# Kernel tuning notes

Hardware: AMD Instinct MI355X
Metric: run time of the kernel (lower is better)

## Reference

```python
import jax, jax.numpy as jnp
import numpy as np

N_HEADS = 4


def setup_inputs() -> dict:
    key = jax.random.key(0)
    k1, k2, k3 = jax.random.split(key, 3)
    B, C, H, W = 16, 512, 32, 32
    x = jax.random.normal(k1, (B, C, H, W), dtype=jnp.float32)
    # Linear weights stored as (in, out) so y = x @ w + b
    w_proj = jax.random.normal(k2, (C, 3 * C), dtype=jnp.float32) * (C ** -0.5)
    b_proj = jnp.zeros((3 * C,), dtype=jnp.float32)
    w_out = jax.random.normal(k3, (C, C), dtype=jnp.float32) * (C ** -0.5)
    b_out = jnp.zeros((C,), dtype=jnp.float32)
    return {"x": x, "w_proj": w_proj, "b_proj": b_proj, "w_out": w_out, "b_out": b_out}


def reference(x, w_proj, b_proj, w_out, b_out):
    B, C, H, W = x.shape
    d_k = C // N_HEADS
    scale = d_k ** -0.5
    # NOTE: original module defines GroupNorm but never applies it in forward.
    xf = x.reshape(B, C, H * W).transpose(0, 2, 1)          # (B, N, C)
    qkv = xf @ w_proj + b_proj                                # (B, N, 3C)
    qkv = qkv.reshape(B, -1, N_HEADS, 3 * d_k)
    q, k, v = jnp.split(qkv, 3, axis=-1)                      # each (B, N, H, d_k)
    attn = jnp.einsum('bihd,bjhd->bijh', q, k) * scale        # (B, N, N, H)
    attn = jax.nn.softmax(attn, axis=2)                       # softmax over j
    res = jnp.einsum('bijh,bjhd->bihd', attn, v)              # (B, N, H, d_k)
    res = res.reshape(B, -1, N_HEADS * d_k)                   # (B, N, C)
    res = res @ w_out + b_out + xf                            # residual add
    return res.transpose(0, 2, 1).reshape(B, C, H, W)
```

## Files before the change

kernel.cpp:

```cpp
#include <hip/hip_runtime.h>

#define B_  16
#define C_  512
#define N_  1024
#define NH  4
#define DK  128
#define M3  1536

typedef unsigned short u16;
typedef unsigned int   u32;
typedef __attribute__((ext_vector_type(8))) short bfrag;
typedef __attribute__((ext_vector_type(4))) float f4;

#define MFMA(a, b, c) __builtin_amdgcn_mfma_f32_16x16x32_bf16(a, b, c, 0, 0, 0)

#define GL2LDS(gp, lp) __builtin_amdgcn_global_load_lds( \
    (__attribute__((address_space(1))) const unsigned int*)(const void*)(gp), \
    (__attribute__((address_space(3))) unsigned int*)(void*)(lp), 16, 0, 0)

__device__ __forceinline__ u16 f2bf(float f) {
    u32 u = __float_as_uint(f);
    return (u16)((u + 0x7FFFu + ((u >> 16) & 1u)) >> 16);
}
__device__ __forceinline__ float bf2f(u16 h) { return __uint_as_float(((u32)h) << 16); }

#define QSCL 0.12751741859316937f

__global__ __launch_bounds__(256) void conv_split_t(
    const float* __restrict__ src, u16* __restrict__ dhi, u16* __restrict__ dlo,
    int R, int Cc)
{
    __shared__ float Ts[64][65];
    const int tid = threadIdx.x;
    const int c0 = blockIdx.x * 64, r0 = blockIdx.y * 64;
    const size_t bofs = (size_t)blockIdx.z * R * Cc;

#pragma unroll
    for (int p = 0; p < 4; ++p) {
        int r = p * 16 + (tid >> 4);
        int c = (tid & 15) * 4;
        float4 v = *(const float4*)(src + bofs + (size_t)(r0 + r) * Cc + c0 + c);
        Ts[c + 0][r] = v.x; Ts[c + 1][r] = v.y; Ts[c + 2][r] = v.z; Ts[c + 3][r] = v.w;
    }
    __syncthreads();
#pragma unroll
    for (int p = 0; p < 4; ++p) {
        int cc = p * 16 + (tid >> 4);
        int rr = (tid & 15) * 4;
        float f0 = Ts[cc][rr + 0], f1 = Ts[cc][rr + 1];
        float f2 = Ts[cc][rr + 2], f3 = Ts[cc][rr + 3];
        u16 h0 = f2bf(f0), h1 = f2bf(f1), h2 = f2bf(f2), h3 = f2bf(f3);
        u16 l0 = f2bf(f0 - bf2f(h0)), l1 = f2bf(f1 - bf2f(h1));
        u16 l2 = f2bf(f2 - bf2f(h2)), l3 = f2bf(f3 - bf2f(h3));
        size_t o = bofs + (size_t)(c0 + cc) * R + r0 + rr;
        *(uint2*)(void*)(dhi + o) = make_uint2((u32)h0 | ((u32)h1 << 16), (u32)h2 | ((u32)h3 << 16));
        *(uint2*)(void*)(dlo + o) = make_uint2((u32)l0 | ((u32)l1 << 16), (u32)l2 | ((u32)l3 << 16));
    }
}

__global__ __launch_bounds__(256, 2) void qkv_mfma(
    const u16* __restrict__ xt_hi, const u16* __restrict__ xt_lo,
    const u16* __restrict__ wpT_hi, const u16* __restrict__ wpT_lo,
    const float* __restrict__ bp,
    u16* __restrict__ Qh, u16* __restrict__ Ql,
    u16* __restrict__ Kh, u16* __restrict__ Kl,
    u16* __restrict__ Vth, u16* __restrict__ Vtl)
{
    __shared__ __align__(16) u16 AH[128 * 64], AL[128 * 64], BH[128 * 64], BL[128 * 64];
    const int tid = threadIdx.x;
    const int l = tid & 63, w = tid >> 6;
    const int wr = w >> 1, wc = w & 1;
    const int lm = l & 15, kg = l >> 4;
    const int bx = blockIdx.x, by = blockIdx.y, b = blockIdx.z;
    const int m0 = bx * 128, n0 = by * 128;

    const u16* gsrc =
        (w == 0) ? xt_hi + ((size_t)b * N_ + n0) * C_ :
        (w == 1) ? xt_lo + ((size_t)b * N_ + n0) * C_ :
        (w == 2) ? wpT_hi + (size_t)m0 * C_ :
                   wpT_lo + (size_t)m0 * C_;
    u16* ldst = (w == 0) ? AH : (w == 1) ? AL : (w == 2) ? BH : BL;
    const int lane_off = (l >> 3) * C_ + (((l & 7) ^ (l >> 3)) << 3);

    f4 acc[4][4] = {};

    for (int it = 0; it < 8; ++it) {
        __syncthreads();
        const u16* g = gsrc + it * 64 + lane_off;
#pragma unroll
        for (int u = 0; u < 16; ++u)
            GL2LDS(g + (size_t)u * 8 * C_, ldst + u * 512);
        __syncthreads();

#pragma unroll
        for (int kk = 0; kk < 2; ++kk) {
            bfrag ah[4], al[4], bh[4], bl[4];
            const int s = ((kk * 4 + kg) ^ (lm & 7)) << 3;
#pragma unroll
            for (int f = 0; f < 4; ++f) {
                const int ar = wr * 64 + f * 16 + lm;
                const int br = wc * 64 + f * 16 + lm;
                ah[f] = *(const bfrag*)(AH + ar * 64 + s);
                al[f] = *(const bfrag*)(AL + ar * 64 + s);
                bh[f] = *(const bfrag*)(BH + br * 64 + s);
                bl[f] = *(const bfrag*)(BL + br * 64 + s);
            }
#pragma unroll
            for (int i = 0; i < 4; ++i)
#pragma unroll
                for (int j = 0; j < 4; ++j) {
                    acc[i][j] = MFMA(ah[i], bh[j], acc[i][j]);
                    acc[i][j] = MFMA(ah[i], bl[j], acc[i][j]);
                    acc[i][j] = MFMA(al[i], bh[j], acc[i][j]);
                }
        }
    }

    const int hh = bx / 3, t = bx - hh * 3;
#pragma unroll
    for (int j = 0; j < 4; ++j) {
        const int mcol = m0 + wc * 64 + j * 16 + lm;
        const float bias = bp[mcol];
        const int d = mcol & 127;
#pragma unroll
        for (int i = 0; i < 4; ++i) {
            const int tok = n0 + wr * 64 + i * 16 + kg * 4;
            if (t == 2) {
                u16 hb[4], lb[4];
#pragma unroll
                for (int r = 0; r < 4; ++r) {
                    float v = acc[i][j][r] + bias;
                    hb[r] = f2bf(v);
                    lb[r] = f2bf(v - bf2f(hb[r]));
                }
                const size_t o = ((size_t)(b * NH + hh) * DK + d) * N_ + tok;
                *(uint2*)(void*)(Vth + o) = make_uint2((u32)hb[0] | ((u32)hb[1] << 16),
                                                       (u32)hb[2] | ((u32)hb[3] << 16));
                *(uint2*)(void*)(Vtl + o) = make_uint2((u32)lb[0] | ((u32)lb[1] << 16),
                                                       (u32)lb[2] | ((u32)lb[3] << 16));
            } else {
                u16* dh = (t == 0) ? Qh : Kh;
                u16* dl = (t == 0) ? Ql : Kl;
                const size_t o = ((size_t)(b * NH + hh) * N_ + tok) * DK + d;
#pragma unroll
                for (int r = 0; r < 4; ++r) {
                    float v = acc[i][j][r] + bias;
                    if (t == 0) v *= QSCL;
                    u16 hb = f2bf(v);
                    dh[o + (size_t)r * DK] = hb;
                    dl[o + (size_t)r * DK] = f2bf(v - bf2f(hb));
                }
            }
        }
    }
}

__global__ __launch_bounds__(512, 2) void attn_mfma(
    const u16* __restrict__ Qh_, const u16* __restrict__ Ql_,
    const u16* __restrict__ Kh_, const u16* __restrict__ Kl_,
    const u16* __restrict__ Vth_, const u16* __restrict__ Vtl_,
    u16* __restrict__ res_hi, u16* __restrict__ res_lo)
{
    __shared__ __align__(16) u16 KH[64 * 128], KL[64 * 128];
    __shared__ __align__(16) u16 VH[128 * 64], VL[128 * 64];
    __shared__ u16 Ph[8][2][16][72], Pl[8][2][16][72];

    const int tid = threadIdx.x;
    const int l = tid & 63, w = tid >> 6;
    const int lm = l & 15, kg = l >> 4;
    const int bh = blockIdx.x;
    const int qc = blockIdx.y;
    const int i0s = qc * 256 + w * 16 + lm;
    const size_t head = (size_t)bh * N_ * DK;

    const u16* sgK = (w & 2) ? Kl_ : Kh_;
    const u16* sgV = (w & 2) ? Vtl_ : Vth_;
    u16* sdK = (w & 2) ? KL : KH;
    u16* sdV = (w & 2) ? VL : VH;
    const int sub0 = (w & 1) * 8;

    bfrag qfh[2][4], qfl[2][4];
#pragma unroll
    for (int s = 0; s < 2; ++s) {
        const u16* qp  = Qh_ + head + (size_t)(i0s + s * 128) * DK + kg * 8;
        const u16* qp2 = Ql_ + head + (size_t)(i0s + s * 128) * DK + kg * 8;
#pragma unroll
        for (int kc = 0; kc < 4; ++kc) {
            qfh[s][kc] = *(const bfrag*)(qp + kc * 32);
            qfl[s][kc] = *(const bfrag*)(qp2 + kc * 32);
        }
    }

    f4 acc_o[2][8] = {};
    float m_r[2] = {-3.0e38f, -3.0e38f}, l_r[2] = {0.f, 0.f};

    for (int jt = 0; jt < 16; ++jt) {
        __syncthreads();
        if (w < 4) {
#pragma unroll
            for (int u = 0; u < 8; ++u) {
                const int rbase = (sub0 + u) * 4;
                const int row = rbase + (l >> 4);
                GL2LDS(sgK + head + (size_t)(jt * 64 + row) * DK + (((l & 15) ^ (row & 7)) << 3),
                       sdK + rbase * 128);
            }
        } else {
#pragma unroll
            for (int u = 0; u < 8; ++u) {
                const int rbase = (sub0 + u) * 8;
                const int row = rbase + (l >> 3);
                GL2LDS(sgV + (size_t)bh * DK * N_ + (size_t)row * N_ + jt * 64
                           + (((l & 7) ^ (row & 7)) << 3),
                       sdV + rbase * 64);
            }
        }
        __syncthreads();

        f4 sacc[2][4] = {};
#pragma unroll
        for (int kc = 0; kc < 4; ++kc) {
#pragma unroll
            for (int jf = 0; jf < 4; ++jf) {
                const int row = jf * 16 + lm;
                const int sw = (((kc << 2) | kg) ^ (lm & 7)) << 3;
                bfrag kh = *(const bfrag*)(KH + row * 128 + sw);
                bfrag kl = *(const bfrag*)(KL + row * 128 + sw);
#pragma unroll
                for (int s = 0; s < 2; ++s) {
                    sacc[s][jf] = MFMA(kh, qfh[s][kc], sacc[s][jf]);
                    sacc[s][jf] = MFMA(kh, qfl[s][kc], sacc[s][jf]);
                    sacc[s][jf] = MFMA(kl, qfh[s][kc], sacc[s][jf]);
                }
            }
        }

#pragma unroll
        for (int s = 0; s < 2; ++s) {
            float mt = sacc[s][0][0];
#pragma unroll
            for (int jf = 0; jf < 4; ++jf)
#pragma unroll
                for (int r = 0; r < 4; ++r) mt = fmaxf(mt, sacc[s][jf][r]);
            mt = fmaxf(mt, __shfl_xor(mt, 16));
            mt = fmaxf(mt, __shfl_xor(mt, 32));
            const float mn = fmaxf(m_r[s], mt);
            const float alpha = exp2f(m_r[s] - mn);
            m_r[s] = mn;

            float rs = 0.f;
#pragma unroll
            for (int jf = 0; jf < 4; ++jf) {
                u16 hb[4], lb[4];
#pragma unroll
                for (int r = 0; r < 4; ++r) {
                    float pv = exp2f(sacc[s][jf][r] - mn);
                    rs += pv;
                    hb[r] = f2bf(pv);
                    lb[r] = f2bf(pv - bf2f(hb[r]));
                }
                *(uint2*)(void*)&Ph[w][s][lm][jf * 16 + kg * 4] =
                    make_uint2((u32)hb[0] | ((u32)hb[1] << 16), (u32)hb[2] | ((u32)hb[3] << 16));
                *(uint2*)(void*)&Pl[w][s][lm][jf * 16 + kg * 4] =
                    make_uint2((u32)lb[0] | ((u32)lb[1] << 16), (u32)lb[2] | ((u32)lb[3] << 16));
            }
            rs += __shfl_xor(rs, 16);
            rs += __shfl_xor(rs, 32);
            l_r[s] = l_r[s] * alpha + rs;
#pragma unroll
            for (int df = 0; df < 8; ++df)
#pragma unroll
                for (int r = 0; r < 4; ++r) acc_o[s][df][r] *= alpha;
        }

#pragma unroll
        for (int kc2 = 0; kc2 < 2; ++kc2) {
            bfrag pbh0 = *(const bfrag*)&Ph[w][0][lm][kc2 * 32 + kg * 8];
            bfrag pbl0 = *(const bfrag*)&Pl[w][0][lm][kc2 * 32 + kg * 8];
            bfrag pbh1 = *(const bfrag*)&Ph[w][1][lm][kc2 * 32 + kg * 8];
            bfrag pbl1 = *(const bfrag*)&Pl[w][1][lm][kc2 * 32 + kg * 8];
#pragma unroll
            for (int df = 0; df < 8; ++df) {
                const int row = df * 16 + lm;
                const int sw = (((kc2 << 2) | kg) ^ (lm & 7)) << 3;
                bfrag vh = *(const bfrag*)(VH + row * 64 + sw);
                bfrag vl = *(const bfrag*)(VL + row * 64 + sw);
                acc_o[0][df] = MFMA(vh, pbh0, acc_o[0][df]);
                acc_o[0][df] = MFMA(vh, pbl0, acc_o[0][df]);
                acc_o[0][df] = MFMA(vl, pbh0, acc_o[0][df]);
                acc_o[1][df] = MFMA(vh, pbh1, acc_o[1][df]);
                acc_o[1][df] = MFMA(vh, pbl1, acc_o[1][df]);
                acc_o[1][df] = MFMA(vl, pbh1, acc_o[1][df]);
            }
        }
    }

    const int b = bh >> 2, h = bh & 3;
#pragma unroll
    for (int s = 0; s < 2; ++s) {
        const float inv = 1.f / l_r[s];
        const size_t ro = ((size_t)b * N_ + i0s + s * 128) * C_ + h * DK;
#pragma unroll
        for (int df = 0; df < 8; ++df) {
            u16 hb[4], lb[4];
#pragma unroll
            for (int r = 0; r < 4; ++r) {
                float v = acc_o[s][df][r] * inv;
                hb[r] = f2bf(v);
                lb[r] = f2bf(v - bf2f(hb[r]));
            }
            const size_t o = ro + df * 16 + kg * 4;
            *(uint2*)(void*)(res_hi + o) = make_uint2((u32)hb[0] | ((u32)hb[1] << 16),
                                                      (u32)hb[2] | ((u32)hb[3] << 16));
            *(uint2*)(void*)(res_lo + o) = make_uint2((u32)lb[0] | ((u32)lb[1] << 16),
                                                      (u32)lb[2] | ((u32)lb[3] << 16));
        }
    }
}

__global__ __launch_bounds__(256, 2) void out_mfma(
    const u16* __restrict__ woT_hi, const u16* __restrict__ woT_lo,
    const u16* __restrict__ res_hi, const u16* __restrict__ res_lo,
    const float* __restrict__ bo, const float* __restrict__ x,
    float* __restrict__ out)
{
    __shared__ __align__(16) u16 AH[128 * 64], AL[128 * 64], BH[128 * 64], BL[128 * 64];
    const int tid = threadIdx.x;
    const int l = tid & 63, w = tid >> 6;
    const int wr = w >> 1, wc = w & 1;
    const int lm = l & 15, kg = l >> 4;
    const int bx = blockIdx.x, by = blockIdx.y, b = blockIdx.z;
    const int c0 = bx * 128, n0 = by * 128;

    const u16* gsrc =
        (w == 0) ? woT_hi + (size_t)c0 * C_ :
        (w == 1) ? woT_lo + (size_t)c0 * C_ :
        (w == 2) ? res_hi + ((size_t)b * N_ + n0) * C_ :
                   res_lo + ((size_t)b * N_ + n0) * C_;
    u16* ldst = (w == 0) ? AH : (w == 1) ? AL : (w == 2) ? BH : BL;
    const int lane_off = (l >> 3) * C_ + (((l & 7) ^ (l >> 3)) << 3);

    f4 acc[4][4] = {};

    for (int it = 0; it < 8; ++it) {
        __syncthreads();
        const u16* g = gsrc + it * 64 + lane_off;
#pragma unroll
        for (int u = 0; u < 16; ++u)
            GL2LDS(g + (size_t)u * 8 * C_, ldst + u * 512);
        __syncthreads();

#pragma unroll
        for (int kk = 0; kk < 2; ++kk) {
            bfrag ah[4], al[4], bh[4], bl[4];
            const int s = ((kk * 4 + kg) ^ (lm & 7)) << 3;
#pragma unroll
            for (int f = 0; f < 4; ++f) {
                const int ar = wr * 64 + f * 16 + lm;
                const int br = wc * 64 + f * 16 + lm;
                ah[f] = *(const bfrag*)(AH + ar * 64 + s);
                al[f] = *(const bfrag*)(AL + ar * 64 + s);
                bh[f] = *(const bfrag*)(BH + br * 64 + s);
                bl[f] = *(const bfrag*)(BL + br * 64 + s);
            }
#pragma unroll
            for (int i = 0; i < 4; ++i)
#pragma unroll
                for (int j = 0; j < 4; ++j) {
                    acc[i][j] = MFMA(ah[i], bh[j], acc[i][j]);
                    acc[i][j] = MFMA(ah[i], bl[j], acc[i][j]);
                    acc[i][j] = MFMA(al[i], bh[j], acc[i][j]);
                }
        }
    }

#pragma unroll
    for (int j = 0; j < 4; ++j) {
        const int ncol = n0 + wc * 64 + j * 16 + lm;
#pragma unroll
        for (int i = 0; i < 4; ++i) {
#pragma unroll
            for (int r = 0; r < 4; ++r) {
                const int crow = c0 + wr * 64 + i * 16 + kg * 4 + r;
                const size_t o = ((size_t)b * C_ + crow) * N_ + ncol;
                out[o] = acc[i][j][r] + bo[crow] + x[o];
            }
        }
    }
}

extern "C" void kernel_launch(void* const* d_in, const int* in_sizes, int n_in,
                              void* d_out, int out_size, void* d_ws, size_t ws_size,
                              hipStream_t stream) {
    const float* x  = (const float*)d_in[0];
    const float* wp = (const float*)d_in[1];
    const float* bp = (const float*)d_in[2];
    const float* wo = (const float*)d_in[3];
    const float* bo = (const float*)d_in[4];
    float* out = (float*)d_out;

    const size_t SEG = (size_t)B_ * N_ * C_;
    u16* xt_hi = (u16*)d_ws;
    u16* xt_lo = xt_hi + SEG;
    u16* Qh  = xt_hi + 2 * SEG;
    u16* Ql  = Qh + SEG;
    u16* Kh  = Ql + SEG;
    u16* Kl  = Kh + SEG;
    u16* Vth = Kl + SEG;
    u16* Vtl = Vth + SEG;
    u16* res_hi = xt_hi;
    u16* res_lo = xt_lo;
    u16* woT_hi = Qh;
    u16* woT_lo = woT_hi + C_ * C_;
    u16* wpT_hi = (u16*)d_out;
    u16* wpT_lo = wpT_hi + C_ * M3;

    conv_split_t<<<dim3(16, 8, 16), 256, 0, stream>>>(x, xt_hi, xt_lo, C_, N_);
    conv_split_t<<<dim3(24, 8, 1), 256, 0, stream>>>(wp, wpT_hi, wpT_lo, C_, M3);
    qkv_mfma<<<dim3(12, 8, 16), 256, 0, stream>>>(xt_hi, xt_lo, wpT_hi, wpT_lo, bp,
                                                  Qh, Ql, Kh, Kl, Vth, Vtl);
    attn_mfma<<<dim3(64, 4), 512, 0, stream>>>(Qh, Ql, Kh, Kl, Vth, Vtl, res_hi, res_lo);
    conv_split_t<<<dim3(8, 8, 1), 256, 0, stream>>>(wo, woT_hi, woT_lo, C_, C_);
    out_mfma<<<dim3(4, 8, 16), 256, 0, stream>>>(woT_hi, woT_lo, res_hi, res_lo, bo, x, out);
}
```

Before: 334.6 us.

## Stage QKV epilogue through LDS for coalesced stores; shrink attention tiles to raise occupancy

The QKV GEMM epilogue now writes biased results into a padded float LDS buffer and then emits 16-byte vectorized hi/lo bf16 stores per row, replacing scattered 2-byte stores to Q/K. The attention kernel moves from 512-thread blocks with 256 queries and 64-key tiles to 256-thread blocks with 128 queries and 32-key tiles, doubling the grid to 512 blocks and cutting LDS per block. Softmax max/sum shuffles are interleaved across the two query sub-tiles. The trade-off is twice as many K/V tile iterations and barriers per block and lower K/V reuse, in exchange for more blocks per CU and better load balance.

```diff
diff --git a/kernel.cpp b/kernel.cpp
--- a/kernel.cpp
+++ b/kernel.cpp
@@ -66,7 +66,13 @@
     u16* __restrict__ Kh, u16* __restrict__ Kl,
     u16* __restrict__ Vth, u16* __restrict__ Vtl)
 {
-    __shared__ __align__(16) u16 AH[128 * 64], AL[128 * 64], BH[128 * 64], BL[128 * 64];
+    __shared__ __align__(16) u32 SMEM[16512];
+    u16* AH = (u16*)SMEM;
+    u16* AL = AH + 128 * 64;
+    u16* BH = AL + 128 * 64;
+    u16* BL = BH + 128 * 64;
+    float* FB = (float*)SMEM;
+
     const int tid = threadIdx.x;
     const int l = tid & 63, w = tid >> 6;
     const int wr = w >> 1, wc = w & 1;
@@ -117,73 +123,82 @@
     }
 
     const int hh = bx / 3, t = bx - hh * 3;
-#pragma unroll
-    for (int j = 0; j < 4; ++j) {
-        const int mcol = m0 + wc * 64 + j * 16 + lm;
-        const float bias = bp[mcol];
-        const int d = mcol & 127;
-#pragma unroll
-        for (int i = 0; i < 4; ++i) {
-            const int tok = n0 + wr * 64 + i * 16 + kg * 4;
-            if (t == 2) {
-                u16 hb[4], lb[4];
+    __syncthreads();
+    {
+        float bias_j[4];
+#pragma unroll
+        for (int j = 0; j < 4; ++j) bias_j[j] = bp[m0 + wc * 64 + j * 16 + lm];
+#pragma unroll
+        for (int j = 0; j < 4; ++j) {
+            const int col = wc * 64 + j * 16 + lm;
+#pragma unroll
+            for (int i = 0; i < 4; ++i) {
 #pragma unroll
                 for (int r = 0; r < 4; ++r) {
-                    float v = acc[i][j][r] + bias;
-                    hb[r] = f2bf(v);
-                    lb[r] = f2bf(v - bf2f(hb[r]));
+                    const int tok = wr * 64 + i * 16 + kg * 4 + r;
+                    float v = acc[i][j][r] + bias_j[j];
+                    if (t == 0) v *= QSCL;
+                    if (t == 2) FB[col * 129 + tok] = v;
+                    else        FB[tok * 129 + col] = v;
                 }
-                const size_t o = ((size_t)(b * NH + hh) * DK + d) * N_ + tok;
-                *(uint2*)(void*)(Vth + o) = make_uint2((u32)hb[0] | ((u32)hb[1] << 16),
-                                                       (u32)hb[2] | ((u32)hb[3] << 16));
-                *(uint2*)(void*)(Vtl + o) = make_uint2((u32)lb[0] | ((u32)lb[1] << 16),
-                                                       (u32)lb[2] | ((u32)lb[3] << 16));
-            } else {
-                u16* dh = (t == 0) ? Qh : Kh;
-                u16* dl = (t == 0) ? Ql : Kl;
-                const size_t o = ((size_t)(b * NH + hh) * N_ + tok) * DK + d;
-#pragma unroll
-                for (int r = 0; r < 4; ++r) {
-                    float v = acc[i][j][r] + bias;
-                    if (t == 0) v *= QSCL;
-                    u16 hb = f2bf(v);
-                    dh[o + (size_t)r * DK] = hb;
-                    dl[o + (size_t)r * DK] = f2bf(v - bf2f(hb));
-                }
-            }
-        }
-    }
-}
-
-__global__ __launch_bounds__(512, 2) void attn_mfma(
+            }
+        }
+    }
+    __syncthreads();
+    {
+        const int r2 = tid >> 1, h = tid & 1;
+        const float* src = FB + r2 * 129 + h * 64;
+        u16* dsth; u16* dstl; size_t o;
+        if (t == 2) {
+            dsth = Vth; dstl = Vtl;
+            o = ((size_t)(b * NH + hh) * DK + r2) * N_ + n0 + h * 64;
+        } else {
+            dsth = (t == 0) ? Qh : Kh;
+            dstl = (t == 0) ? Ql : Kl;
+            o = ((size_t)(b * NH + hh) * N_ + n0 + r2) * DK + h * 64;
+        }
+#pragma unroll
+        for (int c0 = 0; c0 < 64; c0 += 8) {
+            u16 hb[8], lb[8];
+#pragma unroll
+            for (int c = 0; c < 8; ++c) {
+                float v = src[c0 + c];
+                hb[c] = f2bf(v);
+                lb[c] = f2bf(v - bf2f(hb[c]));
+            }
+            *(uint4*)(void*)(dsth + o + c0) = make_uint4(
+                (u32)hb[0] | ((u32)hb[1] << 16), (u32)hb[2] | ((u32)hb[3] << 16),
+                (u32)hb[4] | ((u32)hb[5] << 16), (u32)hb[6] | ((u32)hb[7] << 16));
+            *(uint4*)(void*)(dstl + o + c0) = make_uint4(
+                (u32)lb[0] | ((u32)lb[1] << 16), (u32)lb[2] | ((u32)lb[3] << 16),
+                (u32)lb[4] | ((u32)lb[5] << 16), (u32)lb[6] | ((u32)lb[7] << 16));
+        }
+    }
+}
+
+__global__ __launch_bounds__(256, 2) void attn_mfma(
     const u16* __restrict__ Qh_, const u16* __restrict__ Ql_,
     const u16* __restrict__ Kh_, const u16* __restrict__ Kl_,
     const u16* __restrict__ Vth_, const u16* __restrict__ Vtl_,
     u16* __restrict__ res_hi, u16* __restrict__ res_lo)
 {
-    __shared__ __align__(16) u16 KH[64 * 128], KL[64 * 128];
-    __shared__ __align__(16) u16 VH[128 * 64], VL[128 * 64];
-    __shared__ u16 Ph[8][2][16][72], Pl[8][2][16][72];
+    __shared__ __align__(16) u16 KH[32 * 128], KL[32 * 128];
+    __shared__ __align__(16) u16 VH[128 * 32], VL[128 * 32];
+    __shared__ u16 Ph[4][2][16][40], Pl[4][2][16][40];
 
     const int tid = threadIdx.x;
     const int l = tid & 63, w = tid >> 6;
     const int lm = l & 15, kg = l >> 4;
     const int bh = blockIdx.x;
     const int qc = blockIdx.y;
-    const int i0s = qc * 256 + w * 16 + lm;
+    const int i0s = qc * 128 + w * 16 + lm;
     const size_t head = (size_t)bh * N_ * DK;
 
-    const u16* sgK = (w & 2) ? Kl_ : Kh_;
-    const u16* sgV = (w & 2) ? Vtl_ : Vth_;
-    u16* sdK = (w & 2) ? KL : KH;
-    u16* sdV = (w & 2) ? VL : VH;
-    const int sub0 = (w & 1) * 8;
-
     bfrag qfh[2][4], qfl[2][4];
 #pragma unroll
     for (int s = 0; s < 2; ++s) {
-        const u16* qp  = Qh_ + head + (size_t)(i0s + s * 128) * DK + kg * 8;
-        const u16* qp2 = Ql_ + head + (size_t)(i0s + s * 128) * DK + kg * 8;
+        const u16* qp  = Qh_ + head + (size_t)(i0s + s * 64) * DK + kg * 8;
+        const u16* qp2 = Ql_ + head + (size_t)(i0s + s * 64) * DK + kg * 8;
 #pragma unroll
         for (int kc = 0; kc < 4; ++kc) {
             qfh[s][kc] = *(const bfrag*)(qp + kc * 32);
@@ -194,33 +209,37 @@
     f4 acc_o[2][8] = {};
     float m_r[2] = {-3.0e38f, -3.0e38f}, l_r[2] = {0.f, 0.f};
 
-    for (int jt = 0; jt < 16; ++jt) {
-        __syncthreads();
-        if (w < 4) {
+    for (int jt = 0; jt < 32; ++jt) {
+        __syncthreads();
+        if (w < 2) {
+            const u16* sg = (w & 1) ? Kl_ : Kh_;
+            u16* sd = (w & 1) ? KL : KH;
 #pragma unroll
             for (int u = 0; u < 8; ++u) {
-                const int rbase = (sub0 + u) * 4;
+                const int rbase = u * 4;
                 const int row = rbase + (l >> 4);
-                GL2LDS(sgK + head + (size_t)(jt * 64 + row) * DK + (((l & 15) ^ (row & 7)) << 3),
-                       sdK + rbase * 128);
+                GL2LDS(sg + head + (size_t)(jt * 32 + row) * DK + (((l & 15) ^ (row & 7)) << 3),
+                       sd + rbase * 128);
             }
         } else {
+            const u16* sg = (w & 1) ? Vtl_ : Vth_;
+            u16* sd = (w & 1) ? VL : VH;
 #pragma unroll
             for (int u = 0; u < 8; ++u) {
-                const int rbase = (sub0 + u) * 8;
-                const int row = rbase + (l >> 3);
-                GL2LDS(sgV + (size_t)bh * DK * N_ + (size_t)row * N_ + jt * 64
-                           + (((l & 7) ^ (row & 7)) << 3),
-                       sdV + rbase * 64);
-            }
-        }
-        __syncthreads();
-
-        f4 sacc[2][4] = {};
+                const int rbase = u * 16;
+                const int row = rbase + (l >> 2);
+                GL2LDS(sg + (size_t)bh * DK * N_ + (size_t)row * N_ + jt * 32
+                           + (((l & 3) ^ (row & 3)) << 3),
+                       sd + rbase * 32);
+            }
+        }
+        __syncthreads();
+
+        f4 sacc[2][2] = {};
 #pragma unroll
         for (int kc = 0; kc < 4; ++kc) {
 #pragma unroll
-            for (int jf = 0; jf < 4; ++jf) {
+            for (int jf = 0; jf < 2; ++jf) {
                 const int row = jf * 16 + lm;
                 const int sw = (((kc << 2) | kg) ^ (lm & 7)) << 3;
                 bfrag kh = *(const bfrag*)(KH + row * 128 + sw);
@@ -234,27 +253,32 @@
             }
         }
 
+        float mt[2], mn[2], alpha[2], rs[2];
 #pragma unroll
         for (int s = 0; s < 2; ++s) {
-            float mt = sacc[s][0][0];
-#pragma unroll
-            for (int jf = 0; jf < 4; ++jf)
-#pragma unroll
-                for (int r = 0; r < 4; ++r) mt = fmaxf(mt, sacc[s][jf][r]);
-            mt = fmaxf(mt, __shfl_xor(mt, 16));
-            mt = fmaxf(mt, __shfl_xor(mt, 32));
-            const float mn = fmaxf(m_r[s], mt);
-            const float alpha = exp2f(m_r[s] - mn);
-            m_r[s] = mn;
-
-            float rs = 0.f;
-#pragma unroll
-            for (int jf = 0; jf < 4; ++jf) {
+            float a = fmaxf(fmaxf(sacc[s][0][0], sacc[s][0][1]),
+                            fmaxf(sacc[s][0][2], sacc[s][0][3]));
+            float bb = fmaxf(fmaxf(sacc[s][1][0], sacc[s][1][1]),
+                             fmaxf(sacc[s][1][2], sacc[s][1][3]));
+            mt[s] = fmaxf(a, bb);
+        }
+        mt[0] = fmaxf(mt[0], __shfl_xor(mt[0], 16));
+        mt[1] = fmaxf(mt[1], __shfl_xor(mt[1], 16));
+        mt[0] = fmaxf(mt[0], __shfl_xor(mt[0], 32));
+        mt[1] = fmaxf(mt[1], __shfl_xor(mt[1], 32));
+#pragma unroll
+        for (int s = 0; s < 2; ++s) {
+            mn[s] = fmaxf(m_r[s], mt[s]);
+            alpha[s] = exp2f(m_r[s] - mn[s]);
+            m_r[s] = mn[s];
+            rs[s] = 0.f;
+#pragma unroll
+            for (int jf = 0; jf < 2; ++jf) {
                 u16 hb[4], lb[4];
 #pragma unroll
                 for (int r = 0; r < 4; ++r) {
-                    float pv = exp2f(sacc[s][jf][r] - mn);
-                    rs += pv;
+                    float pv = exp2f(sacc[s][jf][r] - mn[s]);
+                    rs[s] += pv;
                     hb[r] = f2bf(pv);
                     lb[r] = f2bf(pv - bf2f(hb[r]));
                 }
@@ -263,34 +287,36 @@
                 *(uint2*)(void*)&Pl[w][s][lm][jf * 16 + kg * 4] =
                     make_uint2((u32)lb[0] | ((u32)lb[1] << 16), (u32)lb[2] | ((u32)lb[3] << 16));
             }
-            rs += __shfl_xor(rs, 16);
-            rs += __shfl_xor(rs, 32);
-            l_r[s] = l_r[s] * alpha + rs;
+        }
+        rs[0] += __shfl_xor(rs[0], 16);
+        rs[1] += __shfl_xor(rs[1], 16);
+        rs[0] += __shfl_xor(rs[0], 32);
+        rs[1] += __shfl_xor(rs[1], 32);
+#pragma unroll
+        for (int s = 0; s < 2; ++s) {
+            l_r[s] = l_r[s] * alpha[s] + rs[s];
 #pragma unroll
             for (int df = 0; df < 8; ++df)
 #pragma unroll
-                for (int r = 0; r < 4; ++r) acc_o[s][df][r] *= alpha;
-        }
-
-#pragma unroll
-        for (int kc2 = 0; kc2 < 2; ++kc2) {
-            bfrag pbh0 = *(const bfrag*)&Ph[w][0][lm][kc2 * 32 + kg * 8];
-            bfrag pbl0 = *(const bfrag*)&Pl[w][0][lm][kc2 * 32 + kg * 8];
-            bfrag pbh1 = *(const bfrag*)&Ph[w][1][lm][kc2 * 32 + kg * 8];
-            bfrag pbl1 = *(const bfrag*)&Pl[w][1][lm][kc2 * 32 + kg * 8];
-#pragma unroll
-            for (int df = 0; df < 8; ++df) {
-                const int row = df * 16 + lm;
-                const int sw = (((kc2 << 2) | kg) ^ (lm & 7)) << 3;
-                bfrag vh = *(const bfrag*)(VH + row * 64 + sw);
-                bfrag vl = *(const bfrag*)(VL + row * 64 + sw);
-                acc_o[0][df] = MFMA(vh, pbh0, acc_o[0][df]);
-                acc_o[0][df] = MFMA(vh, pbl0, acc_o[0][df]);
-                acc_o[0][df] = MFMA(vl, pbh0, acc_o[0][df]);
-                acc_o[1][df] = MFMA(vh, pbh1, acc_o[1][df]);
-                acc_o[1][df] = MFMA(vh, pbl1, acc_o[1][df]);
-                acc_o[1][df] = MFMA(vl, pbh1, acc_o[1][df]);
-            }
+                for (int r = 0; r < 4; ++r) acc_o[s][df][r] *= alpha[s];
+        }
+
+        bfrag pbh0 = *(const bfrag*)&Ph[w][0][lm][kg * 8];
+        bfrag pbl0 = *(const bfrag*)&Pl[w][0][lm][kg * 8];
+        bfrag pbh1 = *(const bfrag*)&Ph[w][1][lm][kg * 8];
+        bfrag pbl1 = *(const bfrag*)&Pl[w][1][lm][kg * 8];
+#pragma unroll
+        for (int df = 0; df < 8; ++df) {
+            const int row = df * 16 + lm;
+            const int sw = (kg ^ (lm & 3)) << 3;
+            bfrag vh = *(const bfrag*)(VH + row * 32 + sw);
+            bfrag vl = *(const bfrag*)(VL + row * 32 + sw);
+            acc_o[0][df] = MFMA(vh, pbh0, acc_o[0][df]);
+            acc_o[0][df] = MFMA(vh, pbl0, acc_o[0][df]);
+            acc_o[0][df] = MFMA(vl, pbh0, acc_o[0][df]);
+            acc_o[1][df] = MFMA(vh, pbh1, acc_o[1][df]);
+            acc_o[1][df] = MFMA(vh, pbl1, acc_o[1][df]);
+            acc_o[1][df] = MFMA(vl, pbh1, acc_o[1][df]);
         }
     }
 
@@ -298,7 +324,7 @@
 #pragma unroll
     for (int s = 0; s < 2; ++s) {
         const float inv = 1.f / l_r[s];
-        const size_t ro = ((size_t)b * N_ + i0s + s * 128) * C_ + h * DK;
+        const size_t ro = ((size_t)b * N_ + i0s + s * 64) * C_ + h * DK;
 #pragma unroll
         for (int df = 0; df < 8; ++df) {
             u16 hb[4], lb[4];
@@ -418,7 +444,7 @@
     conv_split_t<<<dim3(24, 8, 1), 256, 0, stream>>>(wp, wpT_hi, wpT_lo, C_, M3);
     qkv_mfma<<<dim3(12, 8, 16), 256, 0, stream>>>(xt_hi, xt_lo, wpT_hi, wpT_lo, bp,
                                                   Qh, Ql, Kh, Kl, Vth, Vtl);
-    attn_mfma<<<dim3(64, 4), 512, 0, stream>>>(Qh, Ql, Kh, Kl, Vth, Vtl, res_hi, res_lo);
+    attn_mfma<<<dim3(64, 8), 256, 0, stream>>>(Qh, Ql, Kh, Kl, Vth, Vtl, res_hi, res_lo);
     conv_split_t<<<dim3(8, 8, 1), 256, 0, stream>>>(wo, woT_hi, woT_lo, C_, C_);
     out_mfma<<<dim3(4, 8, 16), 256, 0, stream>>>(woT_hi, woT_lo, res_hi, res_lo, bo, x, out);
 }
```

Result: slower. 373.9 us (+11.7%).
